# Optimization experiments

Hardware: AMD Instinct MI355X
Metric: run time of the kernel (lower is better)

Reference implementation:

```python
import jax, jax.numpy as jnp
import numpy as np

B, S, D, H = 8, 2048, 768, 12

def setup_inputs() -> dict:
    key = jax.random.key(0)
    kx, km, kk, kq, kv = jax.random.split(key, 5)
    return {
        "x": jax.random.normal(kx, (B, S, D), dtype=jnp.float32),
        "mask": jax.random.randint(km, (B, 1, S), 0, 2, dtype=jnp.int32),
        "key_weight": jax.random.normal(kk, (D, H), dtype=jnp.float32),
        "query_weight": jax.random.normal(kq, (D, H), dtype=jnp.float32),
        "value_weight": jax.random.normal(kv, (D, H), dtype=jnp.float32),
    }

def reference(x, mask, key_weight, query_weight, value_weight):
    scale = 1.0 / (key_weight.shape[-1] ** 0.5)
    k = jnp.einsum('bsd,dh->bsh', x, key_weight)
    q = jnp.einsum('bsd,dh->bsh', x, query_weight)
    v = jnp.einsum('bsd,dh->bsh', x, value_weight)
    # scores: (B, S, T) — full score matrix as in the original
    scores = jnp.einsum('bsh,bth->bst', q, k) * scale
    scores = jnp.where(mask == 0, -jnp.inf, scores)
    attn = jax.nn.softmax(scores, axis=-1)
    return jnp.einsum('bst,bth->bsh', attn, v)
```

## Files before the change

### kernel.cpp

```cpp
#include <hip/hip_runtime.h>
#include <math.h>

#define QSCALE (0.2886751345948129f * 1.4426950408889634f)

#if __has_builtin(__builtin_amdgcn_exp2f)
#define EXP2F(x) __builtin_amdgcn_exp2f(x)
#else
#define EXP2F(x) exp2f(x)
#endif

typedef __attribute__((ext_vector_type(8))) _Float16 half8;
typedef __attribute__((ext_vector_type(4))) _Float16 half4_t;
typedef __attribute__((ext_vector_type(4))) float floatx4;

#define MFMA32F16(a, b, c) __builtin_amdgcn_mfma_f32_16x16x32_f16((a), (b), (c), 0, 0, 0)
#define MFMA16F16(a, b, c) __builtin_amdgcn_mfma_f32_16x16x16f16((a), (b), (c), 0, 0, 0)

static __device__ inline float bperm(float v, int addr_bytes) {
    return __int_as_float(__builtin_amdgcn_ds_bpermute(addr_bytes, __float_as_int(v)));
}

__global__ __launch_bounds__(256)
void prep(const float* __restrict__ Wq, const float* __restrict__ Wk,
          const float* __restrict__ Wv, _Float16* __restrict__ wfh,
          _Float16* __restrict__ wfl)
{
    int t = blockIdx.x * 256 + threadIdx.x;
    if (t >= 4608) return;
    int lane = t & 63;
    int nt   = (t >> 6) % 3;
    int ks   = t / 192;
    const float* W = (nt == 0) ? Wq : (nt == 1) ? Wk : Wv;
    const float scale = (nt == 0) ? QSCALE : 1.0f;
    int col = lane & 15;
    int kq  = lane >> 4;
    half8 hi, lo;
    #pragma unroll
    for (int j = 0; j < 8; ++j) {
        int dim = ks * 32 + kq * 8 + j;
        float f = (col < 12) ? W[dim * 12 + col] * scale : 0.0f;
        _Float16 h = (_Float16)f;
        hi[j] = h;
        lo[j] = (_Float16)(f - (float)h);
    }
    size_t off = ((size_t)(ks * 3 + nt) * 64 + lane) * 8;
    *(half8*)(wfh + off) = hi;
    *(half8*)(wfl + off) = lo;
}

__global__ __launch_bounds__(256, 3)
void qkv_mfma(const float* __restrict__ x, const _Float16* __restrict__ wfh,
              const _Float16* __restrict__ wfl, const int* __restrict__ mask,
              _Float16* __restrict__ qfh, _Float16* __restrict__ qfl,
              _Float16* __restrict__ kfh, _Float16* __restrict__ kfl,
              _Float16* __restrict__ vtf)
{
    __shared__ __align__(16) float smem[3072];
    const int tid  = threadIdx.x;
    const int lane = tid & 63;
    const int w    = tid >> 6;
    const int g    = blockIdx.x;
    const int rowbase = g * 16;
    const int m15 = lane & 15;
    const int q8  = lane >> 4;

    const float* xbase = x + (size_t)(rowbase + m15) * 768 + q8 * 8;
    const half8* WH = (const half8*)wfh;
    const half8* WL = (const half8*)wfl;

    float xv[6][8];
    #pragma unroll
    for (int s = 0; s < 6; ++s) {
        const int ks = w * 6 + s;
        *(float4*)(xv[s])     = *(const float4*)(xbase + ks * 32);
        *(float4*)(xv[s] + 4) = *(const float4*)(xbase + ks * 32 + 4);
    }

    floatx4 acc0 = {0.f, 0.f, 0.f, 0.f};
    floatx4 acc1 = acc0, acc2 = acc0;

    half8 bh[2][3], bl[2][3];
    {
        const int ks = w * 6;
        #pragma unroll
        for (int n = 0; n < 3; ++n) {
            bh[0][n] = WH[(ks * 3 + n) * 64 + lane];
            bl[0][n] = WL[(ks * 3 + n) * 64 + lane];
        }
    }

    #pragma unroll
    for (int s = 0; s < 6; ++s) {
        const int cur = s & 1, nxt = cur ^ 1;
        if (s < 5) {
            const int ksn = w * 6 + s + 1;
            #pragma unroll
            for (int n = 0; n < 3; ++n) {
                bh[nxt][n] = WH[(ksn * 3 + n) * 64 + lane];
                bl[nxt][n] = WL[(ksn * 3 + n) * 64 + lane];
            }
        }
        half8 ah, al;
        #pragma unroll
        for (int j = 0; j < 8; ++j) {
            _Float16 h = (_Float16)xv[s][j];
            ah[j] = h;
            al[j] = (_Float16)(xv[s][j] - (float)h);
        }
        acc0 = MFMA32F16(ah, bh[cur][0], acc0);
        acc1 = MFMA32F16(ah, bh[cur][1], acc1);
        acc2 = MFMA32F16(ah, bh[cur][2], acc2);
        acc0 = MFMA32F16(al, bh[cur][0], acc0);
        acc1 = MFMA32F16(al, bh[cur][1], acc1);
        acc2 = MFMA32F16(al, bh[cur][2], acc2);
        acc0 = MFMA32F16(ah, bl[cur][0], acc0);
        acc1 = MFMA32F16(ah, bl[cur][1], acc1);
        acc2 = MFMA32F16(ah, bl[cur][2], acc2);
    }

    *(floatx4*)(smem + ((w * 3 + 0) * 64 + lane) * 4) = acc0;
    *(floatx4*)(smem + ((w * 3 + 1) * 64 + lane) * 4) = acc1;
    *(floatx4*)(smem + ((w * 3 + 2) * 64 + lane) * 4) = acc2;
    __syncthreads();
    floatx4 tot = {0.f, 0.f, 0.f, 0.f};
    if (w < 3) {
        floatx4 t0 = *(const floatx4*)(smem + ((0 * 3 + w) * 64 + lane) * 4);
        floatx4 t1 = *(const floatx4*)(smem + ((1 * 3 + w) * 64 + lane) * 4);
        floatx4 t2 = *(const floatx4*)(smem + ((2 * 3 + w) * 64 + lane) * 4);
        floatx4 t3 = *(const floatx4*)(smem + ((3 * 3 + w) * 64 + lane) * 4);
        tot = t0 + t1 + t2 + t3;
    }
    __syncthreads();

    _Float16* sh = (_Float16*)smem;
    {
        unsigned* zp = (unsigned*)smem;
        for (int i = tid; i < 1152; i += 256) zp[i] = 0u;
    }
    __syncthreads();

    if (w < 3) {
        const int col = m15;
        const int r0  = q8 * 4;
        int msk[4];
        #pragma unroll
        for (int r = 0; r < 4; ++r) msk[r] = mask[rowbase + r0 + r];
        #pragma unroll
        for (int r = 0; r < 4; ++r) {
            const int row = r0 + r;
            const float val = tot[r];
            if (w == 0) {
                if (col < 12) {
                    int idx = ((col >> 3) * 16 + row) * 8 + (col & 7);
                    _Float16 h = (_Float16)val;
                    sh[idx]       = h;
                    sh[512 + idx] = (_Float16)(val - (float)h);
                }
            } else if (w == 1) {
                if (col < 12 && msk[r]) {
                    int idx = ((col >> 3) * 16 + row) * 8 + (col & 7);
                    _Float16 h = (_Float16)val;
                    sh[1024 + idx] = h;
                    sh[1536 + idx] = (_Float16)(val - (float)h);
                }
            } else {
                if (col < 12) {
                    if (msk[r]) {
                        int idx = ((row >> 2) * 16 + col) * 4 + (row & 3);
                        sh[2048 + idx] = (_Float16)val;
                    }
                } else if (col == 12) {
                    int idx = ((row >> 2) * 16 + 12) * 4 + (row & 3);
                    sh[2048 + idx] = (_Float16)(msk[r] ? 1.f : 0.f);
                }
            }
        }
    }
    __syncthreads();

    const int bb = g >> 7;
    const int tt = g & 127;
    const size_t tb64 = (size_t)(bb * 128 + tt) * 64;
    if (w == 0) {
        ((half8*)qfh)[(size_t)g * 64 + lane] = ((const half8*)(sh))[lane];
        ((half8*)qfl)[(size_t)g * 64 + lane] = ((const half8*)(sh + 512))[lane];
    } else if (w == 1) {
        ((half8*)kfh)[tb64 + lane] = ((const half8*)(sh + 1024))[lane];
        ((half8*)kfl)[tb64 + lane] = ((const half8*)(sh + 1536))[lane];
    } else if (w == 2) {
        ((half4_t*)vtf)[tb64 + lane] = ((const half4_t*)(sh + 2048))[lane];
    }
}

__global__ __launch_bounds__(256)
void attn(const _Float16* __restrict__ qfh, const _Float16* __restrict__ qfl,
          const _Float16* __restrict__ kfh, const _Float16* __restrict__ kfl,
          const _Float16* __restrict__ vtf, float* __restrict__ out)
{
    __shared__ float cm[512];
    __shared__ __align__(16) floatx4 co[512];
    const int tid  = threadIdx.x;
    const int lane = tid & 63;
    const int w    = tid >> 6;
    const int bb   = blockIdx.x & 7;
    const int gl   = blockIdx.x >> 3;
    const int g0   = bb * 128 + gl * 2;
    const int m15  = lane & 15;

    const half8 qh0 = *(const half8*)(qfh + ((size_t)g0 * 64 + lane) * 8);
    const half8 ql0 = *(const half8*)(qfl + ((size_t)g0 * 64 + lane) * 8);
    const half8 qh1 = *(const half8*)(qfh + ((size_t)(g0 + 1) * 64 + lane) * 8);
    const half8 ql1 = *(const half8*)(qfl + ((size_t)(g0 + 1) * 64 + lane) * 8);

    const half8* KH = (const half8*)kfh + (size_t)bb * 128 * 64;
    const half8* KL = (const half8*)kfl + (size_t)bb * 128 * 64;
    const half4_t* VT = (const half4_t*)vtf + (size_t)bb * 128 * 64;

    const int a16 = (lane ^ 16) << 2;
    const int a32 = (lane ^ 32) << 2;
    const int a48 = (lane ^ 48) << 2;

    float m0 = -INFINITY, m1 = -INFINITY;
    floatx4 o0 = {0.f, 0.f, 0.f, 0.f};
    floatx4 o1 = o0;

    int t = w;
    half8 kh = KH[t * 64 + lane];
    half8 kl = KL[t * 64 + lane];
    half4_t va = VT[t * 64 + lane];
    for (; t < 128; t += 4) {
        half8 nkh, nkl; half4_t nva;
        if (t + 4 < 128) {
            nkh = KH[(t + 4) * 64 + lane];
            nkl = KL[(t + 4) * 64 + lane];
            nva = VT[(t + 4) * 64 + lane];
        }
        floatx4 s0 = {0.f, 0.f, 0.f, 0.f};
        floatx4 s1 = s0;
        s0 = MFMA32F16(kh, qh0, s0);
        s1 = MFMA32F16(kh, qh1, s1);
        s0 = MFMA32F16(kl, qh0, s0);
        s1 = MFMA32F16(kl, qh1, s1);
        s0 = MFMA32F16(kh, ql0, s0);
        s1 = MFMA32F16(kh, ql1, s1);
        {
            float pm = fmaxf(fmaxf(s0.x, s0.y), fmaxf(s0.z, s0.w));
            float b1 = bperm(pm, a16);
            float b2 = bperm(pm, a32);
            float b3 = bperm(pm, a48);
            pm = fmaxf(fmaxf(pm, b1), fmaxf(b2, b3));
            float mnew = fmaxf(m0, pm);
            float corr = EXP2F(m0 - mnew);
            o0.x *= corr; o0.y *= corr; o0.z *= corr; o0.w *= corr;
            half4_t pb;
            pb[0] = (_Float16)EXP2F(s0.x - mnew);
            pb[1] = (_Float16)EXP2F(s0.y - mnew);
            pb[2] = (_Float16)EXP2F(s0.z - mnew);
            pb[3] = (_Float16)EXP2F(s0.w - mnew);
            o0 = MFMA16F16(va, pb, o0);
            m0 = mnew;
        }
        {
            float pm = fmaxf(fmaxf(s1.x, s1.y), fmaxf(s1.z, s1.w));
            float b1 = bperm(pm, a16);
            float b2 = bperm(pm, a32);
            float b3 = bperm(pm, a48);
            pm = fmaxf(fmaxf(pm, b1), fmaxf(b2, b3));
            float mnew = fmaxf(m1, pm);
            float corr = EXP2F(m1 - mnew);
            o1.x *= corr; o1.y *= corr; o1.z *= corr; o1.w *= corr;
            half4_t pb;
            pb[0] = (_Float16)EXP2F(s1.x - mnew);
            pb[1] = (_Float16)EXP2F(s1.y - mnew);
            pb[2] = (_Float16)EXP2F(s1.z - mnew);
            pb[3] = (_Float16)EXP2F(s1.w - mnew);
            o1 = MFMA16F16(va, pb, o1);
            m1 = mnew;
        }
        kh = nkh; kl = nkl; va = nva;
    }

    cm[(0 * 4 + w) * 64 + lane] = m0;
    cm[(1 * 4 + w) * 64 + lane] = m1;
    co[(0 * 4 + w) * 64 + lane] = o0;
    co[(1 * 4 + w) * 64 + lane] = o1;
    __syncthreads();
    if (w < 2) {
        const int gi = w;
        float gm = -INFINITY;
        #pragma unroll
        for (int w2 = 0; w2 < 4; ++w2) gm = fmaxf(gm, cm[(gi * 4 + w2) * 64 + lane]);
        floatx4 O = {0.f, 0.f, 0.f, 0.f};
        #pragma unroll
        for (int w2 = 0; w2 < 4; ++w2) {
            float f = EXP2F(cm[(gi * 4 + w2) * 64 + lane] - gm);
            floatx4 ow = co[(gi * 4 + w2) * 64 + lane];
            O.x += ow.x * f; O.y += ow.y * f; O.z += ow.z * f; O.w += ow.w * f;
        }
        float L = bperm(O.x, (48 + m15) << 2);
        float inv = 1.0f / L;
        if ((lane >> 4) < 3) {
            float4 ov = make_float4(O.x * inv, O.y * inv, O.z * inv, O.w * inv);
            *(float4*)(out + ((size_t)(g0 + gi) * 16 + m15) * 12 + (lane >> 4) * 4) = ov;
        }
    }
}

extern "C" void kernel_launch(void* const* d_in, const int* in_sizes, int n_in,
                              void* d_out, int out_size, void* d_ws, size_t ws_size,
                              hipStream_t stream) {
    const float* x    = (const float*)d_in[0];
    const int*   mask = (const int*)  d_in[1];
    const float* Wk   = (const float*)d_in[2];
    const float* Wq   = (const float*)d_in[3];
    const float* Wv   = (const float*)d_in[4];
    float* out = (float*)d_out;

    char* base = (char*)d_ws;
    _Float16* qfh = (_Float16*)(base);
    _Float16* qfl = (_Float16*)(base + (1u << 20));
    _Float16* kfh = (_Float16*)(base + (2u << 20));
    _Float16* kfl = (_Float16*)(base + (3u << 20));
    _Float16* vtf = (_Float16*)(base + (4u << 20));
    _Float16* wfh = (_Float16*)(base + 4718592);
    _Float16* wfl = (_Float16*)(base + 4718592 + 73728);

    prep<<<18, 256, 0, stream>>>(Wq, Wk, Wv, wfh, wfl);
    qkv_mfma<<<1024, 256, 0, stream>>>(x, wfh, wfl, mask, qfh, qfl, kfh, kfl, vtf);
    attn<<<512, 256, 0, stream>>>(qfh, qfl, kfh, kfl, vtf, out);
}
```

Before: 122.2 us.

## Process four query tiles per attention block with eight waves sharing K/V loads

```diff
diff --git a/kernel.cpp b/kernel.cpp
--- a/kernel.cpp
+++ b/kernel.cpp
@@ -59,7 +59,7 @@
     const int tid  = threadIdx.x;
     const int lane = tid & 63;
     const int w    = tid >> 6;
-    const int g    = blockIdx.x;
+    const int g    = ((blockIdx.x & 7) << 7) | (blockIdx.x >> 3);
     const int rowbase = g * 16;
     const int m15 = lane & 15;
     const int q8  = lane >> 4;
@@ -192,25 +192,27 @@
     }
 }
 
-__global__ __launch_bounds__(256)
+__global__ __launch_bounds__(512)
 void attn(const _Float16* __restrict__ qfh, const _Float16* __restrict__ qfl,
           const _Float16* __restrict__ kfh, const _Float16* __restrict__ kfl,
           const _Float16* __restrict__ vtf, float* __restrict__ out)
 {
-    __shared__ float cm[512];
-    __shared__ __align__(16) floatx4 co[512];
+    __shared__ float cm[2048];
+    __shared__ __align__(16) floatx4 co[2048];
     const int tid  = threadIdx.x;
     const int lane = tid & 63;
     const int w    = tid >> 6;
     const int bb   = blockIdx.x & 7;
     const int gl   = blockIdx.x >> 3;
-    const int g0   = bb * 128 + gl * 2;
+    const int g0   = bb * 128 + gl * 4;
     const int m15  = lane & 15;
 
-    const half8 qh0 = *(const half8*)(qfh + ((size_t)g0 * 64 + lane) * 8);
-    const half8 ql0 = *(const half8*)(qfl + ((size_t)g0 * 64 + lane) * 8);
-    const half8 qh1 = *(const half8*)(qfh + ((size_t)(g0 + 1) * 64 + lane) * 8);
-    const half8 ql1 = *(const half8*)(qfl + ((size_t)(g0 + 1) * 64 + lane) * 8);
+    half8 qh[4], ql[4];
+    #pragma unroll
+    for (int gi = 0; gi < 4; ++gi) {
+        qh[gi] = *(const half8*)(qfh + ((size_t)(g0 + gi) * 64 + lane) * 8);
+        ql[gi] = *(const half8*)(qfl + ((size_t)(g0 + gi) * 64 + lane) * 8);
+    }
 
     const half8* KH = (const half8*)kfh + (size_t)bb * 128 * 64;
     const half8* KL = (const half8*)kfl + (size_t)bb * 128 * 64;
@@ -220,81 +222,68 @@
     const int a32 = (lane ^ 32) << 2;
     const int a48 = (lane ^ 48) << 2;
 
-    float m0 = -INFINITY, m1 = -INFINITY;
-    floatx4 o0 = {0.f, 0.f, 0.f, 0.f};
-    floatx4 o1 = o0;
+    float m[4] = {-INFINITY, -INFINITY, -INFINITY, -INFINITY};
+    floatx4 o[4];
+    #pragma unroll
+    for (int gi = 0; gi < 4; ++gi) o[gi] = (floatx4){0.f, 0.f, 0.f, 0.f};
 
     int t = w;
     half8 kh = KH[t * 64 + lane];
     half8 kl = KL[t * 64 + lane];
     half4_t va = VT[t * 64 + lane];
-    for (; t < 128; t += 4) {
+    for (; t < 128; t += 8) {
         half8 nkh, nkl; half4_t nva;
-        if (t + 4 < 128) {
-            nkh = KH[(t + 4) * 64 + lane];
-            nkl = KL[(t + 4) * 64 + lane];
-            nva = VT[(t + 4) * 64 + lane];
-        }
-        floatx4 s0 = {0.f, 0.f, 0.f, 0.f};
-        floatx4 s1 = s0;
-        s0 = MFMA32F16(kh, qh0, s0);
-        s1 = MFMA32F16(kh, qh1, s1);
-        s0 = MFMA32F16(kl, qh0, s0);
-        s1 = MFMA32F16(kl, qh1, s1);
-        s0 = MFMA32F16(kh, ql0, s0);
-        s1 = MFMA32F16(kh, ql1, s1);
-        {
-            float pm = fmaxf(fmaxf(s0.x, s0.y), fmaxf(s0.z, s0.w));
+        if (t + 8 < 128) {
+            nkh = KH[(t + 8) * 64 + lane];
+            nkl = KL[(t + 8) * 64 + lane];
+            nva = VT[(t + 8) * 64 + lane];
+        }
+        floatx4 s[4];
+        #pragma unroll
+        for (int gi = 0; gi < 4; ++gi) s[gi] = (floatx4){0.f, 0.f, 0.f, 0.f};
+        #pragma unroll
+        for (int gi = 0; gi < 4; ++gi) s[gi] = MFMA32F16(kh, qh[gi], s[gi]);
+        #pragma unroll
+        for (int gi = 0; gi < 4; ++gi) s[gi] = MFMA32F16(kl, qh[gi], s[gi]);
+        #pragma unroll
+        for (int gi = 0; gi < 4; ++gi) s[gi] = MFMA32F16(kh, ql[gi], s[gi]);
+        #pragma unroll
+        for (int gi = 0; gi < 4; ++gi) {
+            float pm = fmaxf(fmaxf(s[gi].x, s[gi].y), fmaxf(s[gi].z, s[gi].w));
             float b1 = bperm(pm, a16);
             float b2 = bperm(pm, a32);
             float b3 = bperm(pm, a48);
             pm = fmaxf(fmaxf(pm, b1), fmaxf(b2, b3));
-            float mnew = fmaxf(m0, pm);
-            float corr = EXP2F(m0 - mnew);
-            o0.x *= corr; o0.y *= corr; o0.z *= corr; o0.w *= corr;
+            float mnew = fmaxf(m[gi], pm);
+            float corr = EXP2F(m[gi] - mnew);
+            o[gi].x *= corr; o[gi].y *= corr; o[gi].z *= corr; o[gi].w *= corr;
             half4_t pb;
-            pb[0] = (_Float16)EXP2F(s0.x - mnew);
-            pb[1] = (_Float16)EXP2F(s0.y - mnew);
-            pb[2] = (_Float16)EXP2F(s0.z - mnew);
-            pb[3] = (_Float16)EXP2F(s0.w - mnew);
-            o0 = MFMA16F16(va, pb, o0);
-            m0 = mnew;
-        }
-        {
-            float pm = fmaxf(fmaxf(s1.x, s1.y), fmaxf(s1.z, s1.w));
-            float b1 = bperm(pm, a16);
-            float b2 = bperm(pm, a32);
-            float b3 = bperm(pm, a48);
-            pm = fmaxf(fmaxf(pm, b1), fmaxf(b2, b3));
-            float mnew = fmaxf(m1, pm);
-            float corr = EXP2F(m1 - mnew);
-            o1.x *= corr; o1.y *= corr; o1.z *= corr; o1.w *= corr;
-            half4_t pb;
-            pb[0] = (_Float16)EXP2F(s1.x - mnew);
-            pb[1] = (_Float16)EXP2F(s1.y - mnew);
-            pb[2] = (_Float16)EXP2F(s1.z - mnew);
-            pb[3] = (_Float16)EXP2F(s1.w - mnew);
-            o1 = MFMA16F16(va, pb, o1);
-            m1 = mnew;
+            pb[0] = (_Float16)EXP2F(s[gi].x - mnew);
+            pb[1] = (_Float16)EXP2F(s[gi].y - mnew);
+            pb[2] = (_Float16)EXP2F(s[gi].z - mnew);
+            pb[3] = (_Float16)EXP2F(s[gi].w - mnew);
+            o[gi] = MFMA16F16(va, pb, o[gi]);
+            m[gi] = mnew;
         }
         kh = nkh; kl = nkl; va = nva;
     }
 
-    cm[(0 * 4 + w) * 64 + lane] = m0;
-    cm[(1 * 4 + w) * 64 + lane] = m1;
-    co[(0 * 4 + w) * 64 + lane] = o0;
-    co[(1 * 4 + w) * 64 + lane] = o1;
-    __syncthreads();
-    if (w < 2) {
+    #pragma unroll
+    for (int gi = 0; gi < 4; ++gi) {
+        cm[(gi * 8 + w) * 64 + lane] = m[gi];
+        co[(gi * 8 + w) * 64 + lane] = o[gi];
+    }
+    __syncthreads();
+    if (w < 4) {
         const int gi = w;
         float gm = -INFINITY;
         #pragma unroll
-        for (int w2 = 0; w2 < 4; ++w2) gm = fmaxf(gm, cm[(gi * 4 + w2) * 64 + lane]);
+        for (int w2 = 0; w2 < 8; ++w2) gm = fmaxf(gm, cm[(gi * 8 + w2) * 64 + lane]);
         floatx4 O = {0.f, 0.f, 0.f, 0.f};
         #pragma unroll
-        for (int w2 = 0; w2 < 4; ++w2) {
-            float f = EXP2F(cm[(gi * 4 + w2) * 64 + lane] - gm);
-            floatx4 ow = co[(gi * 4 + w2) * 64 + lane];
+        for (int w2 = 0; w2 < 8; ++w2) {
+            float f = EXP2F(cm[(gi * 8 + w2) * 64 + lane] - gm);
+            floatx4 ow = co[(gi * 8 + w2) * 64 + lane];
             O.x += ow.x * f; O.y += ow.y * f; O.z += ow.z * f; O.w += ow.w * f;
         }
         float L = bperm(O.x, (48 + m15) << 2);
@@ -327,5 +316,5 @@
 
     prep<<<18, 256, 0, stream>>>(Wq, Wk, Wv, wfh, wfl);
     qkv_mfma<<<1024, 256, 0, stream>>>(x, wfh, wfl, mask, qfh, qfl, kfh, kfl, vtf);
-    attn<<<512, 256, 0, stream>>>(qfh, qfl, kfh, kfl, vtf, out);
-}
+    attn<<<256, 512, 0, stream>>>(qfh, qfl, kfh, kfl, vtf, out);
+}
```

Result: faster. 117.7 us (-3.7%).
